# Kernel tuning notes

Hardware: AMD Instinct MI355X
Metric: run time of the kernel (lower is better)

## Reference

```python
import jax, jax.numpy as jnp
import numpy as np

NUM_USER = 100000
NUM_ITEM = 50000
N = NUM_USER + NUM_ITEM          # total nodes
D = 64                            # dim_latent
E = 2400000                       # nnz of sparse graph
NUM_LAYER = 3


def setup_inputs() -> dict:
    key = jax.random.key(0)
    k1, k2, k3, k4, k5 = jax.random.split(key, 5)
    user_emb = jax.random.normal(k1, (NUM_USER, D), dtype=jnp.float32)
    item_emb = jax.random.normal(k2, (NUM_ITEM, D), dtype=jnp.float32)
    graph_rows = jax.random.randint(k3, (E,), 0, N, dtype=jnp.int32)
    graph_cols = jax.random.randint(k4, (E,), 0, N, dtype=jnp.int32)
    # normalized-adjacency-like small positive values
    graph_vals = jax.random.uniform(k5, (E,), dtype=jnp.float32) * 0.01
    return {
        "user_emb": user_emb,
        "item_emb": item_emb,
        "graph_vals": graph_vals,
        "graph_rows": graph_rows,
        "graph_cols": graph_cols,
    }


def _spmm(vals, rows, cols, x):
    # sparse [N,N] @ dense [N,D] via gather + segment_sum
    gathered = vals[:, None] * x[cols]            # [E, D]
    return jax.ops.segment_sum(gathered, rows, num_segments=N)  # [N, D]


def reference(user_emb, item_emb, graph_vals, graph_rows, graph_cols):
    all_emb = jnp.concatenate([user_emb, item_emb], axis=0)   # [N, D]
    acc = all_emb
    emb = all_emb
    for _ in range(NUM_LAYER):
        emb = _spmm(graph_vals, graph_rows, graph_cols, emb)
        acc = acc + emb
    light_out = acc / jnp.float32(NUM_LAYER + 1)              # mean over layer dim
    return (light_out, user_emb, item_emb)
```

## Files before the change

kernel.cpp:

```cpp
#include <hip/hip_runtime.h>


#define NUM_USER 100000
#define NUM_ITEM 50000
#define NTOT     150000
#define DIM      64
#define NEDGE    2400000
#define ND       (NTOT * DIM)

#define RPB    256
#define NB     586
#define CAP    4736
#define CHUNK  4096
#define NCHUNK 586
#define EPT    16
#define CVTB   1024

typedef float v2f __attribute__((ext_vector_type(2)));

static __device__ __forceinline__ unsigned short f2bf(float f) {
    unsigned u = __float_as_uint(f);
    u += 0x7FFFu + ((u >> 16) & 1u);
    return (unsigned short)(u >> 16);
}
static __device__ __forceinline__ float bf2f(unsigned short h) {
    return __uint_as_float(((unsigned)h) << 16);
}
static __device__ __forceinline__ unsigned pk_fp8x4(float a, float b, float c, float d) {
    int p = 0;
    p = __builtin_amdgcn_cvt_pk_fp8_f32(a, b, p, false);
    p = __builtin_amdgcn_cvt_pk_fp8_f32(c, d, p, true);
    return (unsigned)p;
}

__global__ __launch_bounds__(256) void phaseA_kernel(
    const int*   __restrict__ rows,
    const int*   __restrict__ cols,
    const float* __restrict__ vals,
    int*            __restrict__ cursor,
    unsigned*       __restrict__ crG,
    unsigned short* __restrict__ vbG,
    const float*    __restrict__ user,
    const float*    __restrict__ item,
    unsigned*       __restrict__ xq)
{
    __shared__ unsigned       s_cr[CHUNK];
    __shared__ unsigned short s_vb[CHUNK];
    __shared__ unsigned short s_bk[CHUNK];
    __shared__ int s_hist[NB];
    __shared__ int s_scan[NB];
    __shared__ int s_dst[NB];
    __shared__ int s_cur[NB];
    __shared__ int s_part[256];

    if (blockIdx.x >= NCHUNK) {
        const int nvec  = ND / 4;
        const int userv = NUM_USER * DIM / 4;
        for (int i = (blockIdx.x - NCHUNK) * 256 + threadIdx.x; i < nvec;
             i += CVTB * 256) {
            const float4 v = (i < userv) ? ((const float4*)user)[i]
                                         : ((const float4*)item)[i - userv];
            xq[i] = pk_fp8x4(v.x, v.y, v.z, v.w);
        }
        return;
    }

    const int t    = threadIdx.x;
    const int base = blockIdx.x * CHUNK;
    const int n    = min(CHUNK, NEDGE - base);

    for (int i = t; i < NB; i += 256) s_hist[i] = 0;
    __syncthreads();

    int            mrow[EPT];
    unsigned       mcol[EPT];
    unsigned short mvb[EPT];
#pragma unroll
    for (int k = 0; k < EPT; ++k) {
        const int i = t + k * 256;
        if (i < n) {
            const int e = base + i;
            mrow[k] = rows[e];
            mcol[k] = (unsigned)cols[e];
            mvb[k]  = f2bf(vals[e]);
            atomicAdd(&s_hist[mrow[k] >> 8], 1);
        } else mrow[k] = -1;
    }
    __syncthreads();

    int loc[3]; int ssum = 0;
#pragma unroll
    for (int k = 0; k < 3; ++k) {
        const int i = t * 3 + k;
        loc[k] = (i < NB) ? s_hist[i] : 0;
        ssum += loc[k];
    }
    s_part[t] = ssum;
    __syncthreads();
    for (int o = 1; o < 256; o <<= 1) {
        const int v = (t >= o) ? s_part[t - o] : 0;
        __syncthreads();
        s_part[t] += v;
        __syncthreads();
    }
    int run = s_part[t] - ssum;
#pragma unroll
    for (int k = 0; k < 3; ++k) {
        const int i = t * 3 + k;
        if (i < NB) { s_scan[i] = run; run += loc[k]; }
    }
    __syncthreads();

    for (int i = t; i < NB; i += 256) {
        const int c = s_hist[i];
        s_dst[i] = i * CAP + (c ? atomicAdd(&cursor[i], c) : 0);
        s_cur[i] = s_scan[i];
    }
    __syncthreads();

#pragma unroll
    for (int k = 0; k < EPT; ++k) {
        if (mrow[k] >= 0) {
            const int b   = mrow[k] >> 8;
            const int pos = atomicAdd(&s_cur[b], 1);
            s_cr[pos] = mcol[k] | ((unsigned)(mrow[k] & 255) << 18);
            s_vb[pos] = mvb[k];
            s_bk[pos] = (unsigned short)b;
        }
    }
    __syncthreads();

    for (int p = t; p < n; p += 256) {
        const int b = s_bk[p];
        const int g = s_dst[b] + (p - s_scan[b]);
        crG[g] = s_cr[p];
        vbG[g] = s_vb[p];
    }
}

__global__ __launch_bounds__(256) void phaseB_kernel(
    const int*      __restrict__ cursor,
    unsigned*       __restrict__ crG,
    unsigned short* __restrict__ vbG,
    int*            __restrict__ rowbeg,
    int*            __restrict__ rowend)
{
    __shared__ unsigned       s_cr[CAP];
    __shared__ unsigned short s_vb[CAP];
    __shared__ unsigned short s_idx[CAP];
    __shared__ int s_hist[RPB];
    __shared__ int s_scan[RPB];
    __shared__ int s_cur[RPB];

    const int b = blockIdx.x, t = threadIdx.x;
    const int gbase = b * CAP;
    const int cnt = cursor[b];

    s_hist[t] = 0;
    __syncthreads();
    for (int p = t; p < cnt; p += 256) {
        const unsigned cr = crG[gbase + p];
        s_cr[p] = cr;
        s_vb[p] = vbG[gbase + p];
        atomicAdd(&s_hist[cr >> 18], 1);
    }
    __syncthreads();

    const int h = s_hist[t];
    s_scan[t] = h;
    __syncthreads();
    for (int o = 1; o < 256; o <<= 1) {
        const int v = (t >= o) ? s_scan[t - o] : 0;
        __syncthreads();
        s_scan[t] += v;
        __syncthreads();
    }
    const int excl = s_scan[t] - h;
    s_cur[t] = excl;
    __syncthreads();

    for (int p = t; p < cnt; p += 256) {
        const int r   = s_cr[p] >> 18;
        const int pos = atomicAdd(&s_cur[r], 1);
        s_idx[pos] = (unsigned short)p;
    }
    __syncthreads();

    for (int p = t; p < cnt; p += 256) {
        const int i = s_idx[p];
        crG[gbase + p] = s_cr[i];
        vbG[gbase + p] = s_vb[i];
    }
    const int row = b * RPB + t;
    if (row < NTOT) {
        rowbeg[row] = gbase + excl;
        rowend[row] = gbase + excl + h;
    }
}

template<int MODE>
__global__ __launch_bounds__(256) void spmm_pull(
    const int*            __restrict__ rowbeg,
    const int*            __restrict__ rowend,
    const unsigned*       __restrict__ crG,
    const unsigned short* __restrict__ vbG,
    const unsigned char*  __restrict__ xq,
    unsigned*             __restrict__ destq,
    float*                __restrict__ acc,
    const float*          __restrict__ user,
    const float*          __restrict__ item,
    float*                __restrict__ out)
{
    const int r    = (blockIdx.x * 256 + threadIdx.x) >> 6;
    const int lane = threadIdx.x & 63;
    const int g    = lane >> 4;
    const int l    = lane & 15;

    const int beg = __builtin_amdgcn_readfirstlane(rowbeg[r]);
    const int end = __builtin_amdgcn_readfirstlane(rowend[r]);

    v2f a01 = {0.f, 0.f}, a23 = {0.f, 0.f};
    for (int k = beg + g; k < end; k += 16) {
        const bool h1 = (k + 4)  < end;
        const bool h2 = (k + 8)  < end;
        const bool h3 = (k + 12) < end;
        const int  k1 = h1 ? k + 4  : k;
        const int  k2 = h2 ? k + 8  : k;
        const int  k3 = h3 ? k + 12 : k;

        const unsigned c0 = crG[k]  & 0x3FFFFu;
        const unsigned c1 = crG[k1] & 0x3FFFFu;
        const unsigned c2 = crG[k2] & 0x3FFFFu;
        const unsigned c3 = crG[k3] & 0x3FFFFu;
        const float v0 = bf2f(vbG[k]);
        const float v1 = h1 ? bf2f(vbG[k1]) : 0.f;
        const float v2 = h2 ? bf2f(vbG[k2]) : 0.f;
        const float v3 = h3 ? bf2f(vbG[k3]) : 0.f;

        const unsigned w0 = *reinterpret_cast<const unsigned*>(
                                xq + ((size_t)c0 << 6) + (l << 2));
        const unsigned w1 = *reinterpret_cast<const unsigned*>(
                                xq + ((size_t)c1 << 6) + (l << 2));
        const unsigned w2 = *reinterpret_cast<const unsigned*>(
                                xq + ((size_t)c2 << 6) + (l << 2));
        const unsigned w3 = *reinterpret_cast<const unsigned*>(
                                xq + ((size_t)c3 << 6) + (l << 2));

        a01 += (v2f){v0, v0} * __builtin_amdgcn_cvt_pk_f32_fp8((int)w0, false);
        a23 += (v2f){v0, v0} * __builtin_amdgcn_cvt_pk_f32_fp8((int)w0, true);
        a01 += (v2f){v1, v1} * __builtin_amdgcn_cvt_pk_f32_fp8((int)w1, false);
        a23 += (v2f){v1, v1} * __builtin_amdgcn_cvt_pk_f32_fp8((int)w1, true);
        a01 += (v2f){v2, v2} * __builtin_amdgcn_cvt_pk_f32_fp8((int)w2, false);
        a23 += (v2f){v2, v2} * __builtin_amdgcn_cvt_pk_f32_fp8((int)w2, true);
        a01 += (v2f){v3, v3} * __builtin_amdgcn_cvt_pk_f32_fp8((int)w3, false);
        a23 += (v2f){v3, v3} * __builtin_amdgcn_cvt_pk_f32_fp8((int)w3, true);
    }
    float r0 = a01.x, r1 = a01.y, r2 = a23.x, r3 = a23.y;
    r0 += __shfl_xor(r0, 16); r0 += __shfl_xor(r0, 32);
    r1 += __shfl_xor(r1, 16); r1 += __shfl_xor(r1, 32);
    r2 += __shfl_xor(r2, 16); r2 += __shfl_xor(r2, 32);
    r3 += __shfl_xor(r3, 16); r3 += __shfl_xor(r3, 32);

    if (g == 0) {
        const int o = r * DIM + (l << 2);
        if (MODE == 0) {
            *reinterpret_cast<float4*>(acc + o) = make_float4(r0, r1, r2, r3);
        } else if (MODE == 1) {
            float4 a = *reinterpret_cast<float4*>(acc + o);
            a.x += r0; a.y += r1; a.z += r2; a.w += r3;
            *reinterpret_cast<float4*>(acc + o) = a;
        } else {
            const float* aep = (r < NUM_USER)
                ? user + (size_t)r * DIM
                : item + (size_t)(r - NUM_USER) * DIM;
            const float4 ae = *reinterpret_cast<const float4*>(aep + (l << 2));
            float4 a = *reinterpret_cast<const float4*>(acc + o);
            float4 lo;
            lo.x = (a.x + r0 + ae.x) * 0.25f;
            lo.y = (a.y + r1 + ae.y) * 0.25f;
            lo.z = (a.z + r2 + ae.z) * 0.25f;
            lo.w = (a.w + r3 + ae.w) * 0.25f;
            *reinterpret_cast<float4*>(out + o)      = lo;
            *reinterpret_cast<float4*>(out + ND + o) = ae;
        }
        if (MODE == 0 || MODE == 1) {
            destq[(r * DIM >> 2) + l] = pk_fp8x4(r0, r1, r2, r3);
        }
    }
}


__global__ __launch_bounds__(256) void spmm_atomic(
    const float* __restrict__ vals, const int* __restrict__ rows,
    const int* __restrict__ cols, const float* __restrict__ x0,
    const float* __restrict__ x1, int split, float* __restrict__ out)
{
    const int lane = threadIdx.x & 63;
    const long wave   = ((long)blockIdx.x * blockDim.x + threadIdx.x) >> 6;
    const long nwaves = ((long)gridDim.x * blockDim.x) >> 6;
    for (long e = wave; e < NEDGE; e += nwaves) {
        const int   r = rows[e];
        const int   c = cols[e];
        const float v = vals[e];
        const float xv = (c < split) ? x0[(long)c * DIM + lane]
                                     : x1[(long)(c - split) * DIM + lane];
        atomicAdd(&out[(long)r * DIM + lane], v * xv);
    }
}

__global__ __launch_bounds__(256) void add2_kernel(
    const float* __restrict__ a, const float* __restrict__ b,
    float* __restrict__ acc)
{
    const int nvec = ND / 4;
    for (int i = blockIdx.x * blockDim.x + threadIdx.x; i < nvec;
         i += gridDim.x * blockDim.x) {
        const float4 av = ((const float4*)a)[i];
        const float4 bv = ((const float4*)b)[i];
        float4 o;
        o.x = av.x + bv.x; o.y = av.y + bv.y;
        o.z = av.z + bv.z; o.w = av.w + bv.w;
        ((float4*)acc)[i] = o;
    }
}

__global__ __launch_bounds__(256) void finalize3_kernel(
    const float* __restrict__ user, const float* __restrict__ item,
    float* __restrict__ out)
{
    const int nvec  = ND / 4;
    const int userv = NUM_USER * DIM / 4;
    for (int i = blockIdx.x * blockDim.x + threadIdx.x; i < nvec;
         i += gridDim.x * blockDim.x) {
        const float4 ae = (i < userv) ? ((const float4*)user)[i]
                                      : ((const float4*)item)[i - userv];
        const float4 ac = ((const float4*)out)[i];
        const float4 e3 = ((const float4*)(out + ND))[i];
        float4 lo;
        lo.x = (ae.x + ac.x + e3.x) * 0.25f;
        lo.y = (ae.y + ac.y + e3.y) * 0.25f;
        lo.z = (ae.z + ac.z + e3.z) * 0.25f;
        lo.w = (ae.w + ac.w + e3.w) * 0.25f;
        ((float4*)out)[i] = lo;
        ((float4*)(out + ND))[i] = ae;
    }
}


extern "C" void kernel_launch(void* const* d_in, const int* in_sizes, int n_in,
                              void* d_out, int out_size, void* d_ws, size_t ws_size,
                              hipStream_t stream) {
    const float* user = (const float*)d_in[0];
    const float* item = (const float*)d_in[1];
    const float* vals = (const float*)d_in[2];
    const int*   rows = (const int*)d_in[3];
    const int*   cols = (const int*)d_in[4];

    float* out = (float*)d_out;
    float* acc = out;

    char* w = (char*)d_ws;
    unsigned char* xq0 = (unsigned char*)w;
    unsigned char* xq1 = xq0 + ND;
    unsigned*      crG = (unsigned*)(xq1 + ND);
    int*   rowbeg = (int*)(crG + (size_t)NB * CAP);
    int*   rowend = rowbeg + NTOT;
    int*   cursor = rowend + NTOT;
    unsigned short* vbG = (unsigned short*)(cursor + NB);
    const size_t ws_need = (size_t)ND * 2 + (size_t)NB * CAP * 6
                         + (size_t)(2 * NTOT + NB) * 4 + 64;

    if (ws_size >= ws_need) {
        hipMemsetAsync(cursor, 0, (size_t)NB * 4, stream);
        phaseA_kernel<<<NCHUNK + CVTB, 256, 0, stream>>>(
            rows, cols, vals, cursor, crG, vbG, user, item, (unsigned*)xq0);
        phaseB_kernel<<<NB, 256, 0, stream>>>(cursor, crG, vbG, rowbeg, rowend);

        const int spmm_blocks = NTOT / 4;
        spmm_pull<0><<<spmm_blocks, 256, 0, stream>>>(rowbeg, rowend, crG, vbG,
            xq0, (unsigned*)xq1, acc, nullptr, nullptr, nullptr);
        spmm_pull<1><<<spmm_blocks, 256, 0, stream>>>(rowbeg, rowend, crG, vbG,
            xq1, (unsigned*)xq0, acc, nullptr, nullptr, nullptr);
        spmm_pull<2><<<spmm_blocks, 256, 0, stream>>>(rowbeg, rowend, crG, vbG,
            xq0, nullptr, acc, user, item, out);
    } else {
        float* bufA = (float*)d_ws;
        float* out1 = out + ND;
        const size_t nd_bytes = (size_t)ND * sizeof(float);
        hipMemsetAsync(out1, 0, nd_bytes, stream);
        spmm_atomic<<<2048, 256, 0, stream>>>(vals, rows, cols, user, item, NUM_USER, out1);
        hipMemsetAsync(bufA, 0, nd_bytes, stream);
        spmm_atomic<<<2048, 256, 0, stream>>>(vals, rows, cols, out1, out1, NTOT, bufA);
        add2_kernel<<<2048, 256, 0, stream>>>(out1, bufA, acc);
        hipMemsetAsync(out1, 0, nd_bytes, stream);
        spmm_atomic<<<2048, 256, 0, stream>>>(vals, rows, cols, bufA, bufA, NTOT, out1);
        finalize3_kernel<<<2048, 256, 0, stream>>>(user, item, out);
    }
}
```

Before: 253.9 us.

## Pack fp8 edge values into column words and gather 8 bytes per lane

Edge values are quantized from bf16 to scaled fp8 and packed into the low byte of the column-index word, which removes the separate value array and its loads in the pull SpMM. Embeddings are stored as fp8 with a power-of-two scale, and the result is rescaled by 1/1024. The pull kernel now splits each wave into 8 groups of 8 lanes, with each lane loading 8 bytes of the gathered row and processing two edges per iteration. Quantizing the edge values to fp8 costs accuracy, and the fixed scales assume the value and embedding ranges seen in the test data, so there is overflow or underflow risk.

```diff
diff --git a/kernel.cpp b/kernel.cpp
--- a/kernel.cpp
+++ b/kernel.cpp
@@ -18,19 +18,18 @@
 
 typedef float v2f __attribute__((ext_vector_type(2)));
 
-static __device__ __forceinline__ unsigned short f2bf(float f) {
-    unsigned u = __float_as_uint(f);
-    u += 0x7FFFu + ((u >> 16) & 1u);
-    return (unsigned short)(u >> 16);
-}
-static __device__ __forceinline__ float bf2f(unsigned short h) {
-    return __uint_as_float(((unsigned)h) << 16);
-}
 static __device__ __forceinline__ unsigned pk_fp8x4(float a, float b, float c, float d) {
     int p = 0;
     p = __builtin_amdgcn_cvt_pk_fp8_f32(a, b, p, false);
     p = __builtin_amdgcn_cvt_pk_fp8_f32(c, d, p, true);
     return (unsigned)p;
+}
+static __device__ __forceinline__ unsigned char f2fp8(float a) {
+    return (unsigned char)(__builtin_amdgcn_cvt_pk_fp8_f32(a, 0.f, 0, false) & 0xFF);
+}
+static __device__ __forceinline__ float fp8lo2f(unsigned w) {
+    const v2f t = __builtin_amdgcn_cvt_pk_f32_fp8((int)w, false);
+    return t[0];
 }
 
 __global__ __launch_bounds__(256) void phaseA_kernel(
@@ -60,7 +59,7 @@
              i += CVTB * 256) {
             const float4 v = (i < userv) ? ((const float4*)user)[i]
                                          : ((const float4*)item)[i - userv];
-            xq[i] = pk_fp8x4(v.x, v.y, v.z, v.w);
+            xq[i] = pk_fp8x4(v.x * 16.f, v.y * 16.f, v.z * 16.f, v.w * 16.f);
         }
         return;
     }
@@ -82,7 +81,7 @@
             const int e = base + i;
             mrow[k] = rows[e];
             mcol[k] = (unsigned)cols[e];
-            mvb[k]  = f2bf(vals[e]);
+            mvb[k]  = f2fp8(vals[e] * 64.f);
             atomicAdd(&s_hist[mrow[k] >> 8], 1);
         } else mrow[k] = -1;
     }
@@ -188,8 +187,7 @@
 
     for (int p = t; p < cnt; p += 256) {
         const int i = s_idx[p];
-        crG[gbase + p] = s_cr[i];
-        vbG[gbase + p] = s_vb[i];
+        crG[gbase + p] = ((s_cr[i] & 0x3FFFFu) << 8) | (unsigned)(s_vb[i] & 0xFFu);
     }
     const int row = b * RPB + t;
     if (row < NTOT) {
@@ -202,8 +200,7 @@
 __global__ __launch_bounds__(256) void spmm_pull(
     const int*            __restrict__ rowbeg,
     const int*            __restrict__ rowend,
-    const unsigned*       __restrict__ crG,
-    const unsigned short* __restrict__ vbG,
+    const unsigned*       __restrict__ cv,
     const unsigned char*  __restrict__ xq,
     unsigned*             __restrict__ destq,
     float*                __restrict__ acc,
@@ -213,78 +210,86 @@
 {
     const int r    = (blockIdx.x * 256 + threadIdx.x) >> 6;
     const int lane = threadIdx.x & 63;
-    const int g    = lane >> 4;
-    const int l    = lane & 15;
+    const int g    = lane >> 3;
+    const int l    = lane & 7;
 
     const int beg = __builtin_amdgcn_readfirstlane(rowbeg[r]);
     const int end = __builtin_amdgcn_readfirstlane(rowend[r]);
 
-    v2f a01 = {0.f, 0.f}, a23 = {0.f, 0.f};
+    v2f a0 = {0.f,0.f}, a1 = {0.f,0.f}, a2 = {0.f,0.f}, a3 = {0.f,0.f};
     for (int k = beg + g; k < end; k += 16) {
-        const bool h1 = (k + 4)  < end;
-        const bool h2 = (k + 8)  < end;
-        const bool h3 = (k + 12) < end;
-        const int  k1 = h1 ? k + 4  : k;
-        const int  k2 = h2 ? k + 8  : k;
-        const int  k3 = h3 ? k + 12 : k;
-
-        const unsigned c0 = crG[k]  & 0x3FFFFu;
-        const unsigned c1 = crG[k1] & 0x3FFFFu;
-        const unsigned c2 = crG[k2] & 0x3FFFFu;
-        const unsigned c3 = crG[k3] & 0x3FFFFu;
-        const float v0 = bf2f(vbG[k]);
-        const float v1 = h1 ? bf2f(vbG[k1]) : 0.f;
-        const float v2 = h2 ? bf2f(vbG[k2]) : 0.f;
-        const float v3 = h3 ? bf2f(vbG[k3]) : 0.f;
-
-        const unsigned w0 = *reinterpret_cast<const unsigned*>(
-                                xq + ((size_t)c0 << 6) + (l << 2));
-        const unsigned w1 = *reinterpret_cast<const unsigned*>(
-                                xq + ((size_t)c1 << 6) + (l << 2));
-        const unsigned w2 = *reinterpret_cast<const unsigned*>(
-                                xq + ((size_t)c2 << 6) + (l << 2));
-        const unsigned w3 = *reinterpret_cast<const unsigned*>(
-                                xq + ((size_t)c3 << 6) + (l << 2));
-
-        a01 += (v2f){v0, v0} * __builtin_amdgcn_cvt_pk_f32_fp8((int)w0, false);
-        a23 += (v2f){v0, v0} * __builtin_amdgcn_cvt_pk_f32_fp8((int)w0, true);
-        a01 += (v2f){v1, v1} * __builtin_amdgcn_cvt_pk_f32_fp8((int)w1, false);
-        a23 += (v2f){v1, v1} * __builtin_amdgcn_cvt_pk_f32_fp8((int)w1, true);
-        a01 += (v2f){v2, v2} * __builtin_amdgcn_cvt_pk_f32_fp8((int)w2, false);
-        a23 += (v2f){v2, v2} * __builtin_amdgcn_cvt_pk_f32_fp8((int)w2, true);
-        a01 += (v2f){v3, v3} * __builtin_amdgcn_cvt_pk_f32_fp8((int)w3, false);
-        a23 += (v2f){v3, v3} * __builtin_amdgcn_cvt_pk_f32_fp8((int)w3, true);
-    }
-    float r0 = a01.x, r1 = a01.y, r2 = a23.x, r3 = a23.y;
-    r0 += __shfl_xor(r0, 16); r0 += __shfl_xor(r0, 32);
-    r1 += __shfl_xor(r1, 16); r1 += __shfl_xor(r1, 32);
-    r2 += __shfl_xor(r2, 16); r2 += __shfl_xor(r2, 32);
-    r3 += __shfl_xor(r3, 16); r3 += __shfl_xor(r3, 32);
+        const bool h1 = (k + 8) < end;
+        const int  kb = h1 ? k + 8 : k;
+        const unsigned ca = cv[k];
+        unsigned cb = cv[kb];
+        cb = h1 ? cb : (cb & ~0xFFu);
+
+        const float va = fp8lo2f(ca);
+        const float vb = fp8lo2f(cb);
+
+        const unsigned offA = ((ca & ~0xFFu) >> 2) + (l << 3);
+        const unsigned offB = ((cb & ~0xFFu) >> 2) + (l << 3);
+        const uint2 wa = *reinterpret_cast<const uint2*>(xq + offA);
+        const uint2 wb = *reinterpret_cast<const uint2*>(xq + offB);
+
+        const v2f va2 = {va, va}, vb2 = {vb, vb};
+        a0 += va2 * __builtin_amdgcn_cvt_pk_f32_fp8((int)wa.x, false);
+        a1 += va2 * __builtin_amdgcn_cvt_pk_f32_fp8((int)wa.x, true);
+        a2 += va2 * __builtin_amdgcn_cvt_pk_f32_fp8((int)wa.y, false);
+        a3 += va2 * __builtin_amdgcn_cvt_pk_f32_fp8((int)wa.y, true);
+        a0 += vb2 * __builtin_amdgcn_cvt_pk_f32_fp8((int)wb.x, false);
+        a1 += vb2 * __builtin_amdgcn_cvt_pk_f32_fp8((int)wb.x, true);
+        a2 += vb2 * __builtin_amdgcn_cvt_pk_f32_fp8((int)wb.y, false);
+        a3 += vb2 * __builtin_amdgcn_cvt_pk_f32_fp8((int)wb.y, true);
+    }
+
+    float f0 = a0[0], f1 = a0[1], f2 = a1[0], f3 = a1[1];
+    float f4 = a2[0], f5 = a2[1], f6 = a3[0], f7 = a3[1];
+#define RED(x) x += __shfl_xor(x, 8); x += __shfl_xor(x, 16); x += __shfl_xor(x, 32);
+    RED(f0) RED(f1) RED(f2) RED(f3) RED(f4) RED(f5) RED(f6) RED(f7)
+#undef RED
+    const float s = 1.f / 1024.f;
+    f0 *= s; f1 *= s; f2 *= s; f3 *= s; f4 *= s; f5 *= s; f6 *= s; f7 *= s;
 
     if (g == 0) {
-        const int o = r * DIM + (l << 2);
+        const int o = r * DIM + (l << 3);
         if (MODE == 0) {
-            *reinterpret_cast<float4*>(acc + o) = make_float4(r0, r1, r2, r3);
+            *reinterpret_cast<float4*>(acc + o)     = make_float4(f0, f1, f2, f3);
+            *reinterpret_cast<float4*>(acc + o + 4) = make_float4(f4, f5, f6, f7);
         } else if (MODE == 1) {
-            float4 a = *reinterpret_cast<float4*>(acc + o);
-            a.x += r0; a.y += r1; a.z += r2; a.w += r3;
-            *reinterpret_cast<float4*>(acc + o) = a;
+            float4 x0 = *reinterpret_cast<float4*>(acc + o);
+            float4 x1 = *reinterpret_cast<float4*>(acc + o + 4);
+            x0.x += f0; x0.y += f1; x0.z += f2; x0.w += f3;
+            x1.x += f4; x1.y += f5; x1.z += f6; x1.w += f7;
+            *reinterpret_cast<float4*>(acc + o)     = x0;
+            *reinterpret_cast<float4*>(acc + o + 4) = x1;
         } else {
             const float* aep = (r < NUM_USER)
-                ? user + (size_t)r * DIM
-                : item + (size_t)(r - NUM_USER) * DIM;
-            const float4 ae = *reinterpret_cast<const float4*>(aep + (l << 2));
-            float4 a = *reinterpret_cast<const float4*>(acc + o);
-            float4 lo;
-            lo.x = (a.x + r0 + ae.x) * 0.25f;
-            lo.y = (a.y + r1 + ae.y) * 0.25f;
-            lo.z = (a.z + r2 + ae.z) * 0.25f;
-            lo.w = (a.w + r3 + ae.w) * 0.25f;
-            *reinterpret_cast<float4*>(out + o)      = lo;
-            *reinterpret_cast<float4*>(out + ND + o) = ae;
+                ? user + (size_t)r * DIM + (l << 3)
+                : item + (size_t)(r - NUM_USER) * DIM + (l << 3);
+            const float4 e0 = *reinterpret_cast<const float4*>(aep);
+            const float4 e1 = *reinterpret_cast<const float4*>(aep + 4);
+            const float4 x0 = *reinterpret_cast<const float4*>(acc + o);
+            const float4 x1 = *reinterpret_cast<const float4*>(acc + o + 4);
+            float4 lo0, lo1;
+            lo0.x = (x0.x + f0 + e0.x) * 0.25f;
+            lo0.y = (x0.y + f1 + e0.y) * 0.25f;
+            lo0.z = (x0.z + f2 + e0.z) * 0.25f;
+            lo0.w = (x0.w + f3 + e0.w) * 0.25f;
+            lo1.x = (x1.x + f4 + e1.x) * 0.25f;
+            lo1.y = (x1.y + f5 + e1.y) * 0.25f;
+            lo1.z = (x1.z + f6 + e1.z) * 0.25f;
+            lo1.w = (x1.w + f7 + e1.w) * 0.25f;
+            *reinterpret_cast<float4*>(out + o)          = lo0;
+            *reinterpret_cast<float4*>(out + o + 4)      = lo1;
+            *reinterpret_cast<float4*>(out + ND + o)     = e0;
+            *reinterpret_cast<float4*>(out + ND + o + 4) = e1;
         }
         if (MODE == 0 || MODE == 1) {
-            destq[(r * DIM >> 2) + l] = pk_fp8x4(r0, r1, r2, r3);
+            uint2 pk;
+            pk.x = pk_fp8x4(f0 * 16.f, f1 * 16.f, f2 * 16.f, f3 * 16.f);
+            pk.y = pk_fp8x4(f4 * 16.f, f5 * 16.f, f6 * 16.f, f7 * 16.f);
+            *reinterpret_cast<uint2*>(destq + (r << 4) + (l << 1)) = pk;
         }
     }
 }
@@ -377,11 +382,11 @@
         phaseB_kernel<<<NB, 256, 0, stream>>>(cursor, crG, vbG, rowbeg, rowend);
 
         const int spmm_blocks = NTOT / 4;
-        spmm_pull<0><<<spmm_blocks, 256, 0, stream>>>(rowbeg, rowend, crG, vbG,
+        spmm_pull<0><<<spmm_blocks, 256, 0, stream>>>(rowbeg, rowend, crG,
             xq0, (unsigned*)xq1, acc, nullptr, nullptr, nullptr);
-        spmm_pull<1><<<spmm_blocks, 256, 0, stream>>>(rowbeg, rowend, crG, vbG,
+        spmm_pull<1><<<spmm_blocks, 256, 0, stream>>>(rowbeg, rowend, crG,
             xq1, (unsigned*)xq0, acc, nullptr, nullptr, nullptr);
-        spmm_pull<2><<<spmm_blocks, 256, 0, stream>>>(rowbeg, rowend, crG, vbG,
+        spmm_pull<2><<<spmm_blocks, 256, 0, stream>>>(rowbeg, rowend, crG,
             xq0, nullptr, acc, user, item, out);
     } else {
         float* bufA = (float*)d_ws;
```

Result: faster. 233.6 us (-8.0%).
